# Performance work log

Hardware: AMD Instinct MI355X
Metric: run time of the kernel (lower is better)

Reference implementation:

```python
import jax, jax.numpy as jnp
import numpy as np

NODE = 64
T = 256
M = 2048
IN_SCALE = 1.0


def setup_inputs() -> dict:
    key = jax.random.key(0)
    k1, k2, k3, k4 = jax.random.split(key, 4)
    # nn.Linear-like init: small weights so the 255-step recurrence is stable
    W = jax.random.normal(k1, (T, NODE, NODE), dtype=jnp.float32) * 0.06
    b = jax.random.normal(k2, (T, NODE), dtype=jnp.float32) * 0.01
    noise_embedding = jnp.ones((1, NODE, T), dtype=jnp.float32)
    eps0 = jax.random.normal(k3, (M, NODE), dtype=jnp.float32)   # initial rsample noise
    eps = jax.random.normal(k4, (T - 1, M, NODE), dtype=jnp.float32)  # per-step noise, t=1..T-1
    return {"W": W, "b": b, "noise_embedding": noise_embedding, "eps0": eps0, "eps": eps}


def reference(W, b, noise_embedding, eps0, eps):
    m = eps0.shape[0]
    dtype = eps0.dtype
    m0 = jnp.zeros((m, NODE), dtype)
    s0 = jnp.full((m, NODE), IN_SCALE, dtype)
    x0 = s0 * eps0  # Normal(m0, s0).rsample()

    st_all = jax.nn.softplus(noise_embedding[0].T)  # (T, NODE)

    def step(x_prev, inp):
        Wt, bt, st, et = inp
        mt = x_prev @ Wt.T + bt                       # (M, NODE) coupling layer
        s_full = jnp.broadcast_to(st, (m, NODE))      # repeat over batch
        xt = mt + s_full * et
        return xt, (xt, mt, s_full)

    _, (xs, ms, ss) = jax.lax.scan(step, x0, (W[1:], b[1:], st_all[1:], eps))

    def pack(first, rest):
        seq = jnp.concatenate([first[None], rest], axis=0)  # (T, M, NODE), t ascending
        return jnp.flip(seq, axis=0).transpose(1, 2, 0)     # (M, NODE, T), reversed order

    return pack(x0, xs), pack(m0, ms), pack(s0, ss)
```

## Files before the change

kernel.cpp:

```cpp
#include <hip/hip_runtime.h>
#include <cmath>


typedef __bf16 bf16x8 __attribute__((ext_vector_type(8)));
typedef float f32x4 __attribute__((ext_vector_type(4)));

#define XB_STRIDE 144

#define SWA(row, col) ((row)*64 + ((col) ^ ((((row)) & 7) << 2)))
#define SWP(row, col) ((row)*32 + ((col) ^ ((((row) >> 2) & 7) << 2)))

__device__ __forceinline__ float softplus_f(float z) {
  return (z > 20.0f) ? z : log1pf(expf(z));
}

__global__ void k_wf(const float* __restrict__ W, const float* __restrict__ ne,
                     bf16x8* __restrict__ Wf, float* __restrict__ st,
                     float* __restrict__ stT) {
  int t = blockIdx.x;
  for (int e = threadIdx.x; e < 512; e += blockDim.x) {
    int lane = e & 63;
    int kh = (e >> 6) & 1;
    int nt = e >> 7;
    int q = lane >> 4, n15 = lane & 15;
    int n = nt * 16 + n15;
    int k0 = kh * 32 + q * 8;
    const float* src = W + ((size_t)t * 64 + n) * 64 + k0;
    bf16x8 v;
#pragma unroll
    for (int j = 0; j < 8; ++j) v[j] = (__bf16)src[j];
    Wf[((size_t)(t * 4 + nt) * 2 + kh) * 64 + lane] = v;
  }
  if (threadIdx.x < 64) {
    int n = threadIdx.x;
    float v = (t == 0) ? 1.0f : softplus_f(ne[n * 256 + t]);
    st[n * 256 + t] = v;
    stT[t * 64 + n] = v;
  }
}

__global__ __launch_bounds__(256) void k_prefix(const bf16x8* __restrict__ Wf,
                                                bf16x8* __restrict__ Pf) {
  __shared__ __align__(16) unsigned char Q[64 * XB_STRIDE];
  int b = blockIdx.x;
  int c = b + 1;
  int tid = threadIdx.x;
  int lane = tid & 63, w = tid >> 6;
  int q = lane >> 4, n15 = lane & 15;
  int rbase = w * 16;
  for (int e = tid; e < 4096; e += 256) {
    int r = e >> 6, k = e & 63;
    *(__bf16*)(Q + r * XB_STRIDE + k * 2) = (__bf16)((r == k) ? 1.0f : 0.0f);
  }
  __syncthreads();
  for (int tl = 0; tl < 16; ++tl) {
    int t = c * 16 + tl;
    bf16x8 a0 = *(const bf16x8*)(Q + (rbase + n15) * XB_STRIDE + q * 16);
    bf16x8 a1 = *(const bf16x8*)(Q + (rbase + n15) * XB_STRIDE + 64 + q * 16);
    f32x4 acc[4];
#pragma unroll
    for (int nt = 0; nt < 4; ++nt) {
      bf16x8 b0 = Wf[((size_t)(t * 4 + nt) * 2 + 0) * 64 + lane];
      bf16x8 b1 = Wf[((size_t)(t * 4 + nt) * 2 + 1) * 64 + lane];
      f32x4 z = {0.f, 0.f, 0.f, 0.f};
      z = __builtin_amdgcn_mfma_f32_16x16x32_bf16(a0, b0, z, 0, 0, 0);
      z = __builtin_amdgcn_mfma_f32_16x16x32_bf16(a1, b1, z, 0, 0, 0);
      acc[nt] = z;
    }
#pragma unroll
    for (int nt = 0; nt < 4; ++nt)
#pragma unroll
      for (int reg = 0; reg < 4; ++reg)
        *(__bf16*)(Q + (rbase + 4 * q + reg) * XB_STRIDE + (nt * 16 + n15) * 2) =
            (__bf16)acc[nt][reg];
    __syncthreads();
    for (int e = tid; e < 512; e += 256) {
      int lane2 = e & 63;
      int kh = (e >> 6) & 1;
      int nt = e >> 7;
      int q2 = lane2 >> 4;
      int nn = nt * 16 + (lane2 & 15);
      bf16x8 v;
#pragma unroll
      for (int j = 0; j < 8; ++j)
        v[j] = *(const __bf16*)(Q + (kh * 32 + q2 * 8 + j) * XB_STRIDE + nn * 2);
      Pf[((size_t)(b * 16 + tl) * 8 + nt * 2 + kh) * 64 + lane2] = v;
    }
    __syncthreads();
  }
}

__global__ __launch_bounds__(256) void k_phase1(
    const float* __restrict__ bb, const float* __restrict__ st,
    const float* __restrict__ eps0, const float* __restrict__ eps,
    const bf16x8* __restrict__ Wf, float* __restrict__ xtemp) {
  __shared__ float stab[16][64];
  __shared__ float btab[16][64];
  __shared__ __align__(16) unsigned char xball[4 * 16 * XB_STRIDE];
  __shared__ __align__(16) float xstage[4][16 * 64];
  int tid = threadIdx.x, w = tid >> 6, lane = tid & 63;
  unsigned char* xb = xball + w * 16 * XB_STRIDE;
  float* xs = xstage[w];
  int c = blockIdx.x >> 5;
  int r0 = ((blockIdx.x & 31) * 4 + w) * 16;
  int q = lane >> 4, n15 = lane & 15;
  for (int e = tid; e < 1024; e += 256) {
    int tl = e >> 6, n = e & 63, t = c * 16 + tl;
    stab[tl][n] = st[n * 256 + t];
    btab[tl][n] = bb[t * 64 + n];
  }
  if (c == 0) {
    for (int i = 0; i < 16; ++i) {
      float v = eps0[(size_t)(r0 + i) * 64 + lane];
      *(__bf16*)(xb + i * XB_STRIDE + lane * 2) = (__bf16)v;
      xtemp[((size_t)(r0 + i)) * 64 + lane] = v;
    }
  } else {
    for (int i = 0; i < 16; ++i)
      *(__bf16*)(xb + i * XB_STRIDE + lane * 2) = (__bf16)0.0f;
  }
  __syncthreads();
  int t0 = (c == 0) ? 1 : c * 16;
  int t1 = c * 16 + 15;
  float epc[16], epn[16];
#pragma unroll
  for (int nt = 0; nt < 4; ++nt)
#pragma unroll
    for (int reg = 0; reg < 4; ++reg)
      epc[nt * 4 + reg] =
          eps[((size_t)(t0 - 1) * 2048 + r0 + 4 * q + reg) * 64 + nt * 16 + n15];
  for (int t = t0; t <= t1; ++t) {
    bool more = (t < t1);
    if (more) {
#pragma unroll
      for (int nt = 0; nt < 4; ++nt)
#pragma unroll
        for (int reg = 0; reg < 4; ++reg)
          epn[nt * 4 + reg] =
              eps[((size_t)t * 2048 + r0 + 4 * q + reg) * 64 + nt * 16 + n15];
    }
    bf16x8 a0 = *(const bf16x8*)(xb + n15 * XB_STRIDE + q * 16);
    bf16x8 a1 = *(const bf16x8*)(xb + n15 * XB_STRIDE + 64 + q * 16);
    f32x4 acc[4];
#pragma unroll
    for (int nt = 0; nt < 4; ++nt) {
      bf16x8 b0 = Wf[((size_t)(t * 4 + nt) * 2 + 0) * 64 + lane];
      bf16x8 b1 = Wf[((size_t)(t * 4 + nt) * 2 + 1) * 64 + lane];
      f32x4 z = {0.f, 0.f, 0.f, 0.f};
      z = __builtin_amdgcn_mfma_f32_16x16x32_bf16(a0, b0, z, 0, 0, 0);
      z = __builtin_amdgcn_mfma_f32_16x16x32_bf16(a1, b1, z, 0, 0, 0);
      acc[nt] = z;
    }
    int tl = t - c * 16;
#pragma unroll
    for (int nt = 0; nt < 4; ++nt) {
      int n = nt * 16 + n15;
      float sv = stab[tl][n];
      float bv = btab[tl][n];
#pragma unroll
      for (int reg = 0; reg < 4; ++reg) {
        int row = 4 * q + reg;
        float xn = acc[nt][reg] + bv + sv * epc[nt * 4 + reg];
        xs[SWA(row, n)] = xn;
        *(__bf16*)(xb + row * XB_STRIDE + n * 2) = (__bf16)xn;
      }
    }
    asm volatile("" ::: "memory");
    {
      size_t basef = ((size_t)t * 2048 + r0) * 64 + 4 * lane;
#pragma unroll
      for (int k = 0; k < 4; ++k) {
        int rr = 4 * k + (lane >> 4);
        int cc = 4 * (lane & 15);
        f32x4 v;
#pragma unroll
        for (int j = 0; j < 4; ++j) v[j] = xs[SWA(rr, cc + j)];
        *(f32x4*)(xtemp + basef + 256 * k) = v;
      }
    }
    asm volatile("" ::: "memory");
    if (more) {
#pragma unroll
      for (int i = 0; i < 16; ++i) epc[i] = epn[i];
    }
  }
}

__global__ __launch_bounds__(256) void k_phase2(const bf16x8* __restrict__ Pf,
                                                const float* __restrict__ xtemp,
                                                bf16x8* __restrict__ hA) {
  __shared__ __align__(16) unsigned char hball[4 * 16 * XB_STRIDE];
  int tid = threadIdx.x, w = tid >> 6, lane = tid & 63;
  unsigned char* hb = hball + w * 16 * XB_STRIDE;
  int rtile = blockIdx.x * 4 + w;
  int r0 = rtile * 16;
  int q = lane >> 4, n15 = lane & 15;
  for (int i = 0; i < 16; ++i) {
    float v = xtemp[((size_t)15 * 2048 + r0 + i) * 64 + lane];
    *(__bf16*)(hb + i * XB_STRIDE + lane * 2) = (__bf16)v;
  }
  for (int c = 1; c <= 15; ++c) {
    bf16x8 a0 = *(const bf16x8*)(hb + n15 * XB_STRIDE + q * 16);
    bf16x8 a1 = *(const bf16x8*)(hb + n15 * XB_STRIDE + 64 + q * 16);
    size_t hbase = ((size_t)(c - 1) * 128 + rtile) * 128;
    hA[hbase + lane] = a0;
    hA[hbase + 64 + lane] = a1;
    if (c == 15) break;
    f32x4 acc[4];
#pragma unroll
    for (int nt = 0; nt < 4; ++nt) {
      bf16x8 b0 = Pf[((size_t)((c - 1) * 16 + 15) * 8 + nt * 2 + 0) * 64 + lane];
      bf16x8 b1 = Pf[((size_t)((c - 1) * 16 + 15) * 8 + nt * 2 + 1) * 64 + lane];
      f32x4 z = {0.f, 0.f, 0.f, 0.f};
      z = __builtin_amdgcn_mfma_f32_16x16x32_bf16(a0, b0, z, 0, 0, 0);
      z = __builtin_amdgcn_mfma_f32_16x16x32_bf16(a1, b1, z, 0, 0, 0);
      acc[nt] = z;
    }
#pragma unroll
    for (int nt = 0; nt < 4; ++nt) {
      int n = nt * 16 + n15;
#pragma unroll
      for (int reg = 0; reg < 4; ++reg) {
        int row = 4 * q + reg;
        float tail = xtemp[((size_t)(16 * c + 15) * 2048 + r0 + row) * 64 + n];
        float hn = acc[nt][reg] + tail;
        *(__bf16*)(hb + row * XB_STRIDE + n * 2) = (__bf16)hn;
      }
    }
  }
}

__global__ __launch_bounds__(256) void k_fix(const bf16x8* __restrict__ Pf,
                                             const bf16x8* __restrict__ hA,
                                             float* __restrict__ xtemp) {
  __shared__ __align__(16) float cst[4][16 * 64];
  int tid = threadIdx.x, w = tid >> 6, lane = tid & 63;
  float* cs = cst[w];
  int rtile = (blockIdx.x & 31) * 4 + w;
  int r0 = rtile * 16;
  int ct = blockIdx.x >> 5;
  int c1 = ct >> 4;
  int tl = ct & 15;
  int c = c1 + 1;
  int t = 16 * c + tl;
  int q = lane >> 4, n15 = lane & 15;
  size_t hbase = ((size_t)c1 * 128 + rtile) * 128;
  bf16x8 a0 = hA[hbase + lane];
  bf16x8 a1 = hA[hbase + 64 + lane];
#pragma unroll
  for (int nt = 0; nt < 4; ++nt) {
    bf16x8 b0 = Pf[((size_t)(c1 * 16 + tl) * 8 + nt * 2 + 0) * 64 + lane];
    bf16x8 b1 = Pf[((size_t)(c1 * 16 + tl) * 8 + nt * 2 + 1) * 64 + lane];
    f32x4 z = {0.f, 0.f, 0.f, 0.f};
    z = __builtin_amdgcn_mfma_f32_16x16x32_bf16(a0, b0, z, 0, 0, 0);
    z = __builtin_amdgcn_mfma_f32_16x16x32_bf16(a1, b1, z, 0, 0, 0);
#pragma unroll
    for (int reg = 0; reg < 4; ++reg)
      cs[SWA(4 * q + reg, nt * 16 + n15)] = z[reg];
  }
  asm volatile("" ::: "memory");
  size_t basef = ((size_t)t * 2048 + r0) * 64 + 4 * lane;
#pragma unroll
  for (int k = 0; k < 4; ++k) {
    int rr = 4 * k + (lane >> 4);
    int cc = 4 * (lane & 15);
    f32x4 cv;
#pragma unroll
    for (int j = 0; j < 4; ++j) cv[j] = cs[SWA(rr, cc + j)];
    f32x4 xv = *(const f32x4*)(xtemp + basef + 256 * k);
    xv += cv;
    *(f32x4*)(xtemp + basef + 256 * k) = xv;
  }
}

__global__ __launch_bounds__(256) void k_pack(const float* __restrict__ stT,
                                              const float* __restrict__ eps0,
                                              const float* __restrict__ eps,
                                              const float* __restrict__ xtemp,
                                              float* __restrict__ out) {
  __shared__ __align__(16) float lds[4][64 * 32];
  int tid = threadIdx.x;
  int w = tid >> 6, lane = tid & 63;
  float* wls = lds[w];
  int task = blockIdx.x * 4 + w;
  int tile = task >> 11;
  int mm = task & 2047;
  int tt0 = tile * 32;
  int iblk0 = 224 - tt0;
  int l15 = lane & 15, L = lane >> 4;
  int n0 = 4 * l15;
  f32x4 xr[8], er[8];
#pragma unroll
  for (int r = 0; r < 8; ++r) {
    int t = tt0 + 4 * r + L;
    xr[r] = *(const f32x4*)(xtemp + ((size_t)t * 2048 + mm) * 64 + n0);
    const float* erow = (t == 0) ? (eps0 + (size_t)mm * 64)
                                 : (eps + ((size_t)(t - 1) * 2048 + mm) * 64);
    er[r] = *(const f32x4*)(erow + n0);
  }
#pragma unroll
  for (int r = 0; r < 8; ++r) {
    int t = tt0 + 4 * r + L;
    f32x4 s = *(const f32x4*)(stT + (size_t)t * 64 + n0);
    er[r] = xr[r] - s * er[r];
  }
  int nrd = lane >> 3;
  int crd = (lane & 7) * 4;
  const size_t MSOFF = (size_t)2048 * 64 * 256;
  size_t obase = ((size_t)mm * 64) * 256 + (size_t)(iblk0 + crd);
#pragma unroll
  for (int r = 0; r < 8; ++r) {
    int col = 31 - 4 * r - L;
#pragma unroll
    for (int j = 0; j < 4; ++j) wls[SWP(n0 + j, col)] = xr[r][j];
  }
  asm volatile("" ::: "memory");
#pragma unroll
  for (int jj = 0; jj < 8; ++jj) {
    int nn = 8 * jj + nrd;
    f32x4 v;
#pragma unroll
    for (int j = 0; j < 4; ++j) v[j] = wls[SWP(nn, crd + j)];
    *(f32x4*)(out + obase + (size_t)nn * 256) = v;
  }
  asm volatile("" ::: "memory");
#pragma unroll
  for (int r = 0; r < 8; ++r) {
    int col = 31 - 4 * r - L;
#pragma unroll
    for (int j = 0; j < 4; ++j) wls[SWP(n0 + j, col)] = er[r][j];
  }
  asm volatile("" ::: "memory");
#pragma unroll
  for (int jj = 0; jj < 8; ++jj) {
    int nn = 8 * jj + nrd;
    f32x4 v;
#pragma unroll
    for (int j = 0; j < 4; ++j) v[j] = wls[SWP(nn, crd + j)];
    *(f32x4*)(out + MSOFF + obase + (size_t)nn * 256) = v;
  }
}

__global__ __launch_bounds__(256) void k_s(const float* __restrict__ st,
                                           float* __restrict__ out) {
  int gid = blockIdx.x * 256 + threadIdx.x;
  int i0 = (gid & 63) * 4;
  int n = (gid >> 6) & 63;
  int m = gid >> 12;
  const float4 rv = *(const float4*)(st + n * 256 + 252 - i0);
  f32x4 v = {rv.w, rv.z, rv.y, rv.x};
  *(f32x4*)(out + (size_t)2 * 2048 * 64 * 256 + ((size_t)m * 64 + n) * 256 + i0) = v;
}

extern "C" void kernel_launch(void* const* d_in, const int* in_sizes, int n_in,
                              void* d_out, int out_size, void* d_ws, size_t ws_size,
                              hipStream_t stream) {
  const float* W = (const float*)d_in[0];
  const float* bb = (const float*)d_in[1];
  const float* ne = (const float*)d_in[2];
  const float* eps0 = (const float*)d_in[3];
  const float* eps = (const float*)d_in[4];
  float* out = (float*)d_out;
  char* ws = (char*)d_ws;
  bf16x8* Wf = (bf16x8*)ws;
  float* st = (float*)(ws + (size_t)(2u << 20));
  float* stT = (float*)(ws + (size_t)(2u << 20) + (128u << 10));
  bf16x8* Pf = (bf16x8*)(ws + (size_t)(2u << 20) + (256u << 10));
  bf16x8* hA = (bf16x8*)(ws + (size_t)(4u << 20) + (256u << 10));
  float* xtemp = out + (size_t)2 * 2048 * 64 * 256;

  hipLaunchKernelGGL(k_wf, dim3(256), dim3(256), 0, stream, W, ne, Wf, st, stT);
  hipLaunchKernelGGL(k_prefix, dim3(15), dim3(256), 0, stream, Wf, Pf);
  hipLaunchKernelGGL(k_phase1, dim3(512), dim3(256), 0, stream, bb, st, eps0, eps, Wf, xtemp);
  hipLaunchKernelGGL(k_phase2, dim3(32), dim3(256), 0, stream, Pf, xtemp, hA);
  hipLaunchKernelGGL(k_fix, dim3(7680), dim3(256), 0, stream, Pf, hA, xtemp);
  hipLaunchKernelGGL(k_pack, dim3(4096), dim3(256), 0, stream, stT, eps0, eps, xtemp, out);
  hipLaunchKernelGGL(k_s, dim3(32768), dim3(256), 0, stream, st, out);
}
```

Measured before the change: 664.2 us.

## Fuse chunk-boundary fixup into pack kernel to skip xtemp read-modify-write

The separate fixup kernel, which added the prefix-propagated correction into xtemp, and the transpose/pack kernel are merged into one kernel. Each block now computes the MFMA correction for its 16-row tile and time chunk in registers, adds it to the loaded xtemp values, and writes both x and m outputs through a padded LDS staging buffer. This removes one full read-modify-write pass over the large xtemp buffer and one launch. In exchange it uses block-wide syncs, a new LDS layout with stride 17, and fewer blocks (1024), which may lower occupancy and store coalescing.

New measurement: 684.0 us. 1.03x slower.

```diff
diff --git a/kernel.cpp b/kernel.cpp
--- a/kernel.cpp
+++ b/kernel.cpp
@@ -8,7 +8,7 @@
 #define XB_STRIDE 144
 
 #define SWA(row, col) ((row)*64 + ((col) ^ ((((row)) & 7) << 2)))
-#define SWP(row, col) ((row)*32 + ((col) ^ ((((row) >> 2) & 7) << 2)))
+#define SWB(row, col) ((row)*32 + ((col) ^ ((((row)) & 7) << 2)))
 
 __device__ __forceinline__ float softplus_f(float z) {
   return (z > 20.0f) ? z : log1pf(expf(z));
@@ -230,114 +230,126 @@
   }
 }
 
-__global__ __launch_bounds__(256) void k_fix(const bf16x8* __restrict__ Pf,
-                                             const bf16x8* __restrict__ hA,
-                                             float* __restrict__ xtemp) {
-  __shared__ __align__(16) float cst[4][16 * 64];
+__global__ __launch_bounds__(256) void k_packfix(
+    const bf16x8* __restrict__ Pf, const bf16x8* __restrict__ hA,
+    const float* __restrict__ stT, const float* __restrict__ eps0,
+    const float* __restrict__ eps, const float* __restrict__ xtemp,
+    float* __restrict__ out) {
+  __shared__ float stg[512 * 17];
+  __shared__ float cwb[4][512];
+  const size_t MSOFF = (size_t)2048 * 64 * 256;
   int tid = threadIdx.x, w = tid >> 6, lane = tid & 63;
-  float* cs = cst[w];
-  int rtile = (blockIdx.x & 31) * 4 + w;
-  int r0 = rtile * 16;
-  int ct = blockIdx.x >> 5;
-  int c1 = ct >> 4;
-  int tl = ct & 15;
-  int c = c1 + 1;
-  int t = 16 * c + tl;
+  int mtile = blockIdx.x & 127;
+  int nh = (blockIdx.x >> 7) & 1;
+  int tq = blockIdx.x >> 8;
+  int mm0 = mtile * 16;
+  int rr0 = lane & 7;
+  int cc = 4 * (lane >> 3);
   int q = lane >> 4, n15 = lane & 15;
-  size_t hbase = ((size_t)c1 * 128 + rtile) * 128;
-  bf16x8 a0 = hA[hbase + lane];
-  bf16x8 a1 = hA[hbase + 64 + lane];
-#pragma unroll
-  for (int nt = 0; nt < 4; ++nt) {
-    bf16x8 b0 = Pf[((size_t)(c1 * 16 + tl) * 8 + nt * 2 + 0) * 64 + lane];
-    bf16x8 b1 = Pf[((size_t)(c1 * 16 + tl) * 8 + nt * 2 + 1) * 64 + lane];
-    f32x4 z = {0.f, 0.f, 0.f, 0.f};
-    z = __builtin_amdgcn_mfma_f32_16x16x32_bf16(a0, b0, z, 0, 0, 0);
-    z = __builtin_amdgcn_mfma_f32_16x16x32_bf16(a1, b1, z, 0, 0, 0);
-#pragma unroll
-    for (int reg = 0; reg < 4; ++reg)
-      cs[SWA(4 * q + reg, nt * 16 + n15)] = z[reg];
-  }
-  asm volatile("" ::: "memory");
-  size_t basef = ((size_t)t * 2048 + r0) * 64 + 4 * lane;
-#pragma unroll
-  for (int k = 0; k < 4; ++k) {
-    int rr = 4 * k + (lane >> 4);
-    int cc = 4 * (lane & 15);
-    f32x4 cv;
-#pragma unroll
-    for (int j = 0; j < 4; ++j) cv[j] = cs[SWA(rr, cc + j)];
-    f32x4 xv = *(const f32x4*)(xtemp + basef + 256 * k);
-    xv += cv;
-    *(f32x4*)(xtemp + basef + 256 * k) = xv;
-  }
-}
-
-__global__ __launch_bounds__(256) void k_pack(const float* __restrict__ stT,
-                                              const float* __restrict__ eps0,
-                                              const float* __restrict__ eps,
-                                              const float* __restrict__ xtemp,
-                                              float* __restrict__ out) {
-  __shared__ __align__(16) float lds[4][64 * 32];
-  int tid = threadIdx.x;
-  int w = tid >> 6, lane = tid & 63;
-  float* wls = lds[w];
-  int task = blockIdx.x * 4 + w;
-  int tile = task >> 11;
-  int mm = task & 2047;
-  int tt0 = tile * 32;
-  int iblk0 = 224 - tt0;
-  int l15 = lane & 15, L = lane >> 4;
-  int n0 = 4 * l15;
-  f32x4 xr[8], er[8];
-#pragma unroll
-  for (int r = 0; r < 8; ++r) {
-    int t = tt0 + 4 * r + L;
-    xr[r] = *(const f32x4*)(xtemp + ((size_t)t * 2048 + mm) * 64 + n0);
-    const float* erow = (t == 0) ? (eps0 + (size_t)mm * 64)
-                                 : (eps + ((size_t)(t - 1) * 2048 + mm) * 64);
-    er[r] = *(const f32x4*)(erow + n0);
-  }
-#pragma unroll
-  for (int r = 0; r < 8; ++r) {
-    int t = tt0 + 4 * r + L;
-    f32x4 s = *(const f32x4*)(stT + (size_t)t * 64 + n0);
-    er[r] = xr[r] - s * er[r];
-  }
-  int nrd = lane >> 3;
-  int crd = (lane & 7) * 4;
-  const size_t MSOFF = (size_t)2048 * 64 * 256;
-  size_t obase = ((size_t)mm * 64) * 256 + (size_t)(iblk0 + crd);
-#pragma unroll
-  for (int r = 0; r < 8; ++r) {
-    int col = 31 - 4 * r - L;
-#pragma unroll
-    for (int j = 0; j < 4; ++j) wls[SWP(n0 + j, col)] = xr[r][j];
-  }
-  asm volatile("" ::: "memory");
-#pragma unroll
-  for (int jj = 0; jj < 8; ++jj) {
-    int nn = 8 * jj + nrd;
-    f32x4 v;
-#pragma unroll
-    for (int j = 0; j < 4; ++j) v[j] = wls[SWP(nn, crd + j)];
-    *(f32x4*)(out + obase + (size_t)nn * 256) = v;
-  }
-  asm volatile("" ::: "memory");
-#pragma unroll
-  for (int r = 0; r < 8; ++r) {
-    int col = 31 - 4 * r - L;
-#pragma unroll
-    for (int j = 0; j < 4; ++j) wls[SWP(n0 + j, col)] = er[r][j];
-  }
-  asm volatile("" ::: "memory");
-#pragma unroll
-  for (int jj = 0; jj < 8; ++jj) {
-    int nn = 8 * jj + nrd;
-    f32x4 v;
-#pragma unroll
-    for (int j = 0; j < 4; ++j) v[j] = wls[SWP(nn, crd + j)];
-    *(f32x4*)(out + MSOFF + obase + (size_t)nn * 256) = v;
+  float* cw = cwb[w];
+  const f32x4 zv = {0.f, 0.f, 0.f, 0.f};
+  int frow = tid >> 2, fcq = (tid & 3) * 4;
+  for (int g = 0; g < 4; ++g) {
+    int c = tq * 4 + g;
+    int tb = c * 16;
+    bf16x8 a0, a1;
+    if (c > 0) {
+      size_t hbase = ((size_t)(c - 1) * 128 + mtile) * 128;
+      a0 = hA[hbase + lane];
+      a1 = hA[hbase + 64 + lane];
+    }
+    f32x4 xv[4][2], ev[4][2];
+#pragma unroll
+    for (int j = 0; j < 4; ++j) {
+      int t = tb + w * 4 + j;
+#pragma unroll
+      for (int k = 0; k < 2; ++k) {
+        int row = mm0 + rr0 + 8 * k;
+        xv[j][k] =
+            *(const f32x4*)(xtemp + ((size_t)t * 2048 + row) * 64 + nh * 32 + cc);
+        const float* ep = (t == 0) ? (eps0 + (size_t)row * 64)
+                                   : (eps + ((size_t)(t - 1) * 2048 + row) * 64);
+        ev[j][k] = *(const f32x4*)(ep + nh * 32 + cc);
+      }
+    }
+    f32x4 mv[4][2];
+#pragma unroll
+    for (int j = 0; j < 4; ++j) {
+      int tl = w * 4 + j;
+      int t = tb + tl;
+      f32x4 cv[2];
+      cv[0] = zv;
+      cv[1] = zv;
+      if (c > 0) {
+#pragma unroll
+        for (int ntl = 0; ntl < 2; ++ntl) {
+          bf16x8 b0 =
+              Pf[((size_t)((c - 1) * 16 + tl) * 8 + (2 * nh + ntl) * 2 + 0) * 64 +
+                 lane];
+          bf16x8 b1 =
+              Pf[((size_t)((c - 1) * 16 + tl) * 8 + (2 * nh + ntl) * 2 + 1) * 64 +
+                 lane];
+          f32x4 z = {0.f, 0.f, 0.f, 0.f};
+          z = __builtin_amdgcn_mfma_f32_16x16x32_bf16(a0, b0, z, 0, 0, 0);
+          z = __builtin_amdgcn_mfma_f32_16x16x32_bf16(a1, b1, z, 0, 0, 0);
+#pragma unroll
+          for (int reg = 0; reg < 4; ++reg)
+            cw[SWB(4 * q + reg, ntl * 16 + n15)] = z[reg];
+        }
+        asm volatile("" ::: "memory");
+#pragma unroll
+        for (int k = 0; k < 2; ++k)
+#pragma unroll
+          for (int jj = 0; jj < 4; ++jj)
+            cv[k][jj] = cw[SWB(rr0 + 8 * k, cc + jj)];
+        asm volatile("" ::: "memory");
+      }
+      f32x4 sv = *(const f32x4*)(stT + (size_t)t * 64 + nh * 32 + cc);
+      int colt = 15 - tl;
+#pragma unroll
+      for (int k = 0; k < 2; ++k) {
+        f32x4 xf = xv[j][k] + cv[k];
+        mv[j][k] = xf - sv * ev[j][k];
+#pragma unroll
+        for (int jj = 0; jj < 4; ++jj)
+          stg[((rr0 + 8 * k) * 32 + cc + jj) * 17 + colt] = xf[jj];
+      }
+    }
+    __syncthreads();
+    int ib0 = 240 - 16 * c;
+#pragma unroll
+    for (int it = 0; it < 8; ++it) {
+      int row = frow + 64 * it;
+      int mi = row >> 5, nl = row & 31;
+      size_t ob = ((size_t)(mm0 + mi) * 64 + nh * 32 + nl) * 256 + ib0 + fcq;
+      f32x4 v;
+#pragma unroll
+      for (int jj = 0; jj < 4; ++jj) v[jj] = stg[row * 17 + fcq + jj];
+      *(f32x4*)(out + ob) = v;
+    }
+    __syncthreads();
+#pragma unroll
+    for (int j = 0; j < 4; ++j) {
+      int colt = 15 - (w * 4 + j);
+#pragma unroll
+      for (int k = 0; k < 2; ++k)
+#pragma unroll
+        for (int jj = 0; jj < 4; ++jj)
+          stg[((rr0 + 8 * k) * 32 + cc + jj) * 17 + colt] = mv[j][k][jj];
+    }
+    __syncthreads();
+#pragma unroll
+    for (int it = 0; it < 8; ++it) {
+      int row = frow + 64 * it;
+      int mi = row >> 5, nl = row & 31;
+      size_t ob =
+          MSOFF + ((size_t)(mm0 + mi) * 64 + nh * 32 + nl) * 256 + ib0 + fcq;
+      f32x4 v;
+#pragma unroll
+      for (int jj = 0; jj < 4; ++jj) v[jj] = stg[row * 17 + fcq + jj];
+      *(f32x4*)(out + ob) = v;
+    }
+    __syncthreads();
   }
 }
 
@@ -373,7 +385,6 @@
   hipLaunchKernelGGL(k_prefix, dim3(15), dim3(256), 0, stream, Wf, Pf);
   hipLaunchKernelGGL(k_phase1, dim3(512), dim3(256), 0, stream, bb, st, eps0, eps, Wf, xtemp);
   hipLaunchKernelGGL(k_phase2, dim3(32), dim3(256), 0, stream, Pf, xtemp, hA);
-  hipLaunchKernelGGL(k_fix, dim3(7680), dim3(256), 0, stream, Pf, hA, xtemp);
-  hipLaunchKernelGGL(k_pack, dim3(4096), dim3(256), 0, stream, stT, eps0, eps, xtemp, out);
+  hipLaunchKernelGGL(k_packfix, dim3(1024), dim3(256), 0, stream, Pf, hA, stT, eps0, eps, xtemp, out);
   hipLaunchKernelGGL(k_s, dim3(32768), dim3(256), 0, stream, st, out);
 }
```
